# Optimization experiments

Measured on AMD Instinct MI355X. Metric: run time of the kernel, lower is better.

## Reference

```python
import jax, jax.numpy as jnp
import numpy as np

N, I, H = 16, 128, 128
B, T = 16, 512


def setup_inputs() -> dict:
    key = jax.random.key(0)
    ks = jax.random.split(key, 6)
    stdv = 1.0 / np.sqrt(H)
    return {
        "x": jax.random.normal(ks[0], (B, T, N * I), dtype=jnp.float32),
        "h_0": jax.random.normal(ks[1], (1, B, N * H), dtype=jnp.float32),
        "weight_ih": jax.random.uniform(ks[2], (N, 3 * H, I), jnp.float32, -stdv, stdv),
        "weight_hh": jax.random.uniform(ks[3], (N, 3 * H, H), jnp.float32, -stdv, stdv),
        "bias_ih": jax.random.uniform(ks[4], (N, 3 * H), jnp.float32, -stdv, stdv),
        "bias_hh": jax.random.uniform(ks[5], (N, 3 * H), jnp.float32, -stdv, stdv),
    }


def reference(x, h_0, weight_ih, weight_hh, bias_ih, bias_hh):
    # x: [B, T, N*I] (batch_first)
    b, t, _ = x.shape
    xr = x.reshape(b, t, N, I)
    # Pre-compute all input projections: [B, T, N, 3H]
    gates_x = jnp.einsum('btni,ngi->btng', xr, weight_ih) + bias_ih[None, None]
    h0 = h_0[0].reshape(b, N, H)  # [B, N, H]

    def step(h, gx):
        # h: [B, N, H]; gx: [B, N, 3H]
        gates_h = jnp.einsum('bnh,ngh->bng', h, weight_hh) + bias_hh[None]
        gx_r, gx_z, gx_n = jnp.split(gx, 3, axis=-1)
        gh_r, gh_z, gh_n = jnp.split(gates_h, 3, axis=-1)
        r = jax.nn.sigmoid(gx_r + gh_r)
        z = jax.nn.sigmoid(gx_z + gh_z)
        n = jnp.tanh(gx_n + r * gh_n)
        h_new = (1 - z) * n + z * h
        return h_new, h_new

    # scan over time: gates_x -> [T, B, N, 3H]
    h_last, hs = jax.lax.scan(step, h0, jnp.swapaxes(gates_x, 0, 1))
    output = jnp.swapaxes(hs, 0, 1).reshape(b, t, N * H)  # [B, T, N*H]
    h_n = h_last.reshape(1, b, N * H)
    return output, h_n
```

## Files before the change

### kernel.cpp

```cpp
#include <hip/hip_runtime.h>
#include <cstdint>
#include <cmath>

#define N_HEADS 16
#define I_DIM 128
#define H_DIM 128
#define B_SZ 16
#define T_SZ 512
#define G3 384
#define BT (B_SZ * T_SZ)
#define LDW 136
#define OUT_HN_OFFSET ((size_t)B_SZ * T_SZ * (N_HEADS * H_DIM))
#define CHUNK 8
#define NCHUNK (T_SZ / CHUNK)

typedef __attribute__((ext_vector_type(8))) short bf16x8;
typedef __attribute__((ext_vector_type(4))) float f32x4;

static __device__ __forceinline__ unsigned short f2bf(float f) {
  unsigned int u = __float_as_uint(f);
  unsigned int r = (u + 0x7FFFu + ((u >> 16) & 1u)) >> 16;
  return (unsigned short)r;
}
static __device__ __forceinline__ float bf2f(unsigned short s) {
  return __uint_as_float((unsigned int)s << 16);
}
static __device__ __forceinline__ uint2 pack4(float4 v) {
  uint2 p;
  p.x = (unsigned int)f2bf(v.x) | ((unsigned int)f2bf(v.y) << 16);
  p.y = (unsigned int)f2bf(v.z) | ((unsigned int)f2bf(v.w) << 16);
  return p;
}
static __device__ __forceinline__ bf16x8 pack8(float4 a, float4 b) {
  union { uint2 u[2]; bf16x8 v; } r;
  r.u[0] = pack4(a);
  r.u[1] = pack4(b);
  return r.v;
}

__global__ __launch_bounds__(256) void gates_x_mfma(
    const float* __restrict__ x, const float* __restrict__ w_ih,
    const float* __restrict__ b_ih, unsigned short* __restrict__ gates) {
  const int n = blockIdx.z;
  const int grp = blockIdx.x;
  const int tid = threadIdx.x;
  const int wave = tid >> 6;
  const int lane = tid & 63;
  const int m16 = lane & 15;
  const int quad = lane >> 4;

  extern __shared__ __align__(16) unsigned short lds_pool[];
  unsigned short* Ws = lds_pool;
  unsigned short* Xs = lds_pool + G3 * LDW;

  const int xrow = tid >> 2;
  const int xq = tid & 3;

  float4 xf[8];
  {
    const float4* xg =
        (const float4*)(x + (size_t)(grp * 512 + xrow) * 2048 + n * I_DIM) +
        xq * 8;
#pragma unroll
    for (int i = 0; i < 8; ++i) xf[i] = xg[i];
  }

  {
    const float4* wsrc = (const float4*)(w_ih + (size_t)n * G3 * I_DIM);
#pragma unroll
    for (int i = 0; i < 48; ++i) {
      const int idx = i * 256 + tid;
      *(uint2*)&Ws[(idx >> 5) * LDW + (idx & 31) * 4] = pack4(wsrc[idx]);
    }
  }

  float bias[3][8];
#pragma unroll
  for (int gb = 0; gb < 3; ++gb)
#pragma unroll
    for (int j = 0; j < 8; ++j)
      bias[gb][j] = b_ih[n * G3 + gb * 128 + j * 16 + m16];

  for (int tile = 0; tile < 8; ++tile) {
    const int bt0 = grp * 512 + tile * 64;

    __syncthreads();
#pragma unroll
    for (int i = 0; i < 8; ++i)
      *(uint2*)&Xs[xrow * LDW + xq * 32 + i * 4] = pack4(xf[i]);
    __syncthreads();

    if (tile < 7) {
      const float4* xg =
          (const float4*)(x + (size_t)(bt0 + 64 + xrow) * 2048 + n * I_DIM) +
          xq * 8;
#pragma unroll
      for (int i = 0; i < 8; ++i) xf[i] = xg[i];
    }

#pragma unroll
    for (int gb = 0; gb < 3; ++gb) {
      f32x4 acc[8];
#pragma unroll
      for (int j = 0; j < 8; ++j) acc[j] = (f32x4){0.f, 0.f, 0.f, 0.f};

#pragma unroll
      for (int kt = 0; kt < 4; ++kt) {
        const bf16x8 afrag =
            *(const bf16x8*)&Xs[(wave * 16 + m16) * LDW + kt * 32 + quad * 8];
#pragma unroll
        for (int j = 0; j < 8; ++j) {
          const bf16x8 bfrag =
              *(const bf16x8*)&Ws[(gb * 128 + j * 16 + m16) * LDW + kt * 32 +
                                  quad * 8];
          acc[j] = __builtin_amdgcn_mfma_f32_16x16x32_bf16(afrag, bfrag,
                                                           acc[j], 0, 0, 0);
        }
      }

#pragma unroll
      for (int j = 0; j < 8; ++j) {
        const int g = gb * 128 + j * 16 + m16;
#pragma unroll
        for (int r = 0; r < 4; ++r) {
          const int bt = bt0 + wave * 16 + quad * 4 + r;
          gates[((size_t)n * BT + bt) * G3 + g] =
              f2bf(acc[j][r] + bias[gb][j]);
        }
      }
    }
  }
}

__global__ __launch_bounds__(256, 1) void gru_scan_kernel(
    const float* __restrict__ h0, const float* __restrict__ w_hh,
    const float* __restrict__ b_hh, const unsigned short* __restrict__ gates,
    float* __restrict__ out) {
  const int b = blockIdx.x >> 4;
  const int n = blockIdx.x & 15;
  const int tid = threadIdx.x;
  const int wave = tid >> 6;
  const int lane = tid & 63;
  const int m16 = lane & 15;
  const int quad = lane >> 4;

  __shared__ __align__(16) unsigned short h2[2][2][H_DIM];
  __shared__ __align__(16) unsigned short gbuf[2][CHUNK * G3];

  bf16x8 wf[6][4];
  {
    const int cb0 = 2 * wave;
    const int cbs[6] = {cb0, 8 + cb0, 16 + cb0, cb0 + 1, 9 + cb0, 17 + cb0};
#pragma unroll
    for (int j = 0; j < 6; ++j) {
      const int g = cbs[j] * 16 + m16;
      const float4* wr = (const float4*)(w_hh + ((size_t)n * G3 + g) * H_DIM);
#pragma unroll
      for (int kt = 0; kt < 4; ++kt)
        wf[j][kt] = pack8(wr[kt * 8 + quad * 2], wr[kt * 8 + quad * 2 + 1]);
    }
  }

  const bool upd = quad < 2;
  const int elem = wave * 32 + quad * 16 + m16;

  float bh_r = 0.f, bh_z = 0.f, bh_n = 0.f, h_old = 0.f;
  if (upd) {
    bh_r = b_hh[n * G3 + elem];
    bh_z = b_hh[n * G3 + elem + 128];
    bh_n = b_hh[n * G3 + elem + 256];
    h_old = h0[(size_t)b * 2048 + n * H_DIM + elem];
    const unsigned short hh = f2bf(h_old);
    h2[0][0][elem] = hh;
    h2[0][1][elem] = f2bf(h_old - bf2f(hh));
  }

  const unsigned short* gx_base =
      gates + ((size_t)n * BT + (size_t)b * T_SZ) * G3;
  float* out_base = out + (size_t)b * T_SZ * 2048 + n * H_DIM;

  uint2 pf0, pf1, pf2;
  {
    const uint2* gsrc = (const uint2*)gx_base;
    pf0 = gsrc[tid];
    pf1 = gsrc[256 + tid];
    pf2 = gsrc[512 + tid];
    uint2* gd = (uint2*)gbuf[0];
    gd[tid] = pf0;
    gd[256 + tid] = pf1;
    gd[512 + tid] = pf2;
  }
  __syncthreads();

  float oreg[CHUNK];

  for (int c = 0; c < NCHUNK; ++c) {
    const int gb = c & 1;

    if (c + 1 < NCHUNK) {
      const uint2* gsrc =
          (const uint2*)(gx_base + (size_t)(c + 1) * CHUNK * G3);
      pf0 = gsrc[tid];
      pf1 = gsrc[256 + tid];
      pf2 = gsrc[512 + tid];
    }

#pragma unroll
    for (int s = 0; s < CHUNK; ++s) {
      const int rb = s & 1;
      const int wb = rb ^ 1;

      float gxr = 0.f, gxz = 0.f, gxn = 0.f;
      if (upd) {
        const unsigned short* gx = &gbuf[gb][s * G3 + elem];
        gxr = bf2f(gx[0]);
        gxz = bf2f(gx[128]);
        gxn = bf2f(gx[256]);
      }

      f32x4 acc[6];
#pragma unroll
      for (int j = 0; j < 6; ++j) acc[j] = (f32x4){0.f, 0.f, 0.f, 0.f};
#pragma unroll
      for (int kt = 0; kt < 4; ++kt) {
        const bf16x8 av =
            *(const bf16x8*)&h2[rb][m16 & 1][kt * 32 + quad * 8];
#pragma unroll
        for (int j = 0; j < 6; ++j)
          acc[j] = __builtin_amdgcn_mfma_f32_16x16x32_bf16(av, wf[j][kt],
                                                           acc[j], 0, 0, 0);
      }

      const float s0 = acc[0][0] + acc[0][1];
      const float s1 = acc[1][0] + acc[1][1];
      const float s2 = acc[2][0] + acc[2][1];
      const float s3 = acc[3][0] + acc[3][1];
      const float s4 = acc[4][0] + acc[4][1];
      const float s5 = acc[5][0] + acc[5][1];

      if (upd) {
        const float ghr = (quad ? s3 : s0) + bh_r;
        const float ghz = (quad ? s4 : s1) + bh_z;
        const float ghn = (quad ? s5 : s2) + bh_n;
        const float r = 1.f / (1.f + __expf(-(gxr + ghr)));
        const float z = 1.f / (1.f + __expf(-(gxz + ghz)));
        const float targ = gxn + r * ghn;
        const float e2 = __expf(-2.f * fabsf(targ));
        float nn = (1.f - e2) / (1.f + e2);
        nn = (targ < 0.f) ? -nn : nn;
        const float hn = (1.f - z) * nn + z * h_old;
        const unsigned short hh = f2bf(hn);
        h2[wb][0][elem] = hh;
        h2[wb][1][elem] = f2bf(hn - bf2f(hh));
        h_old = hn;
        oreg[s] = hn;
      }

      if (s == CHUNK - 1 && c + 1 < NCHUNK) {
        uint2* gd = (uint2*)gbuf[gb ^ 1];
        gd[tid] = pf0;
        gd[256 + tid] = pf1;
        gd[512 + tid] = pf2;
      }
      __syncthreads();
    }

    if (upd) {
#pragma unroll
      for (int s = 0; s < CHUNK; ++s)
        out_base[(size_t)(c * CHUNK + s) * 2048 + elem] = oreg[s];
    }
  }

  if (upd) {
    out[OUT_HN_OFFSET + (size_t)b * 2048 + n * H_DIM + elem] = h_old;
  }
}

extern "C" void kernel_launch(void* const* d_in, const int* in_sizes, int n_in,
                              void* d_out, int out_size, void* d_ws,
                              size_t ws_size, hipStream_t stream) {
  const float* x    = (const float*)d_in[0];
  const float* h0   = (const float*)d_in[1];
  const float* w_ih = (const float*)d_in[2];
  const float* w_hh = (const float*)d_in[3];
  const float* b_ih = (const float*)d_in[4];
  const float* b_hh = (const float*)d_in[5];
  float* out = (float*)d_out;
  unsigned short* gates = (unsigned short*)d_ws;

  static bool lds_opt_in = false;
  if (!lds_opt_in) {
    (void)hipFuncSetAttribute(reinterpret_cast<const void*>(&gates_x_mfma),
                              hipFuncAttributeMaxDynamicSharedMemorySize,
                              (G3 + 64) * LDW * (int)sizeof(unsigned short));
    lds_opt_in = true;
  }

  dim3 gridA(16, 1, N_HEADS);
  gates_x_mfma<<<gridA, 256, (G3 + 64) * LDW * sizeof(unsigned short),
                 stream>>>(x, w_ih, b_ih, gates);
  gru_scan_kernel<<<256, 256, 0, stream>>>(h0, w_hh, b_hh, gates, out);
}
```

Before: 421.7 us.

## Transpose gate layout to time-major rows and interleave r/z/n in shared memory

```diff
diff --git a/kernel.cpp b/kernel.cpp
--- a/kernel.cpp
+++ b/kernel.cpp
@@ -121,12 +121,13 @@
 #pragma unroll
       for (int j = 0; j < 8; ++j) {
         const int g = gb * 128 + j * 16 + m16;
-#pragma unroll
-        for (int r = 0; r < 4; ++r) {
-          const int bt = bt0 + wave * 16 + quad * 4 + r;
-          gates[((size_t)n * BT + bt) * G3 + g] =
-              f2bf(acc[j][r] + bias[gb][j]);
-        }
+        float4 v;
+        v.x = acc[j][0] + bias[gb][j];
+        v.y = acc[j][1] + bias[gb][j];
+        v.z = acc[j][2] + bias[gb][j];
+        v.w = acc[j][3] + bias[gb][j];
+        const int bt = bt0 + wave * 16 + quad * 4;
+        *(uint2*)&gates[((size_t)n * G3 + g) * BT + bt] = pack4(v);
       }
     }
   }
@@ -145,7 +146,7 @@
   const int quad = lane >> 4;
 
   __shared__ __align__(16) unsigned short h2[2][2][H_DIM];
-  __shared__ __align__(16) unsigned short gbuf[2][CHUNK * G3];
+  __shared__ __align__(16) unsigned short gbuf[2][CHUNK * 512];
 
   bf16x8 wf[6][4];
   {
@@ -175,34 +176,38 @@
     h2[0][1][elem] = f2bf(h_old - bf2f(hh));
   }
 
-  const unsigned short* gx_base =
-      gates + ((size_t)n * BT + (size_t)b * T_SZ) * G3;
+  const size_t grow0 = ((size_t)n * G3 + tid) * BT + (size_t)b * T_SZ;
+  const size_t grow1 = ((size_t)n * G3 + 256 + tid) * BT + (size_t)b * T_SZ;
+
+  auto scatter = [&](unsigned short* buf, int g, uint4 v) {
+    unsigned short* d = buf + (g & 127) * 4 + (g >> 7);
+    d[0]    = (unsigned short)v.x;
+    d[512]  = (unsigned short)(v.x >> 16);
+    d[1024] = (unsigned short)v.y;
+    d[1536] = (unsigned short)(v.y >> 16);
+    d[2048] = (unsigned short)v.z;
+    d[2560] = (unsigned short)(v.z >> 16);
+    d[3072] = (unsigned short)v.w;
+    d[3584] = (unsigned short)(v.w >> 16);
+  };
+
+  uint4 pfA, pfB;
+  pfA = *(const uint4*)(gates + grow0);
+  if (tid < 128) pfB = *(const uint4*)(gates + grow1);
+  scatter(gbuf[0], tid, pfA);
+  if (tid < 128) scatter(gbuf[0], 256 + tid, pfB);
+  __syncthreads();
+
   float* out_base = out + (size_t)b * T_SZ * 2048 + n * H_DIM;
-
-  uint2 pf0, pf1, pf2;
-  {
-    const uint2* gsrc = (const uint2*)gx_base;
-    pf0 = gsrc[tid];
-    pf1 = gsrc[256 + tid];
-    pf2 = gsrc[512 + tid];
-    uint2* gd = (uint2*)gbuf[0];
-    gd[tid] = pf0;
-    gd[256 + tid] = pf1;
-    gd[512 + tid] = pf2;
-  }
-  __syncthreads();
-
   float oreg[CHUNK];
 
   for (int c = 0; c < NCHUNK; ++c) {
     const int gb = c & 1;
 
     if (c + 1 < NCHUNK) {
-      const uint2* gsrc =
-          (const uint2*)(gx_base + (size_t)(c + 1) * CHUNK * G3);
-      pf0 = gsrc[tid];
-      pf1 = gsrc[256 + tid];
-      pf2 = gsrc[512 + tid];
+      pfA = *(const uint4*)(gates + grow0 + (size_t)(c + 1) * CHUNK);
+      if (tid < 128)
+        pfB = *(const uint4*)(gates + grow1 + (size_t)(c + 1) * CHUNK);
     }
 
 #pragma unroll
@@ -210,44 +215,50 @@
       const int rb = s & 1;
       const int wb = rb ^ 1;
 
-      float gxr = 0.f, gxz = 0.f, gxn = 0.f;
+      uint2 gxu = {0u, 0u};
+      if (upd) gxu = *(const uint2*)&gbuf[gb][s * 512 + elem * 4];
+      const float gxr = __uint_as_float(gxu.x << 16);
+      const float gxz = __uint_as_float(gxu.x & 0xffff0000u);
+      const float gxn = __uint_as_float(gxu.y << 16);
+
+      const unsigned short* hsrc = &h2[rb][m16 & 1][0];
+      const bf16x8 av0 = *(const bf16x8*)&hsrc[0 * 32 + quad * 8];
+      const bf16x8 av1 = *(const bf16x8*)&hsrc[1 * 32 + quad * 8];
+      const bf16x8 av2 = *(const bf16x8*)&hsrc[2 * 32 + quad * 8];
+      const bf16x8 av3 = *(const bf16x8*)&hsrc[3 * 32 + quad * 8];
+
+      f32x4 acc[6];
+#pragma unroll
+      for (int j = 0; j < 6; ++j) acc[j] = (f32x4){0.f, 0.f, 0.f, 0.f};
+#pragma unroll
+      for (int j = 0; j < 6; ++j)
+        acc[j] = __builtin_amdgcn_mfma_f32_16x16x32_bf16(av0, wf[j][0],
+                                                         acc[j], 0, 0, 0);
+#pragma unroll
+      for (int j = 0; j < 6; ++j)
+        acc[j] = __builtin_amdgcn_mfma_f32_16x16x32_bf16(av1, wf[j][1],
+                                                         acc[j], 0, 0, 0);
+#pragma unroll
+      for (int j = 0; j < 6; ++j)
+        acc[j] = __builtin_amdgcn_mfma_f32_16x16x32_bf16(av2, wf[j][2],
+                                                         acc[j], 0, 0, 0);
+#pragma unroll
+      for (int j = 0; j < 6; ++j)
+        acc[j] = __builtin_amdgcn_mfma_f32_16x16x32_bf16(av3, wf[j][3],
+                                                         acc[j], 0, 0, 0);
+
       if (upd) {
-        const unsigned short* gx = &gbuf[gb][s * G3 + elem];
-        gxr = bf2f(gx[0]);
-        gxz = bf2f(gx[128]);
-        gxn = bf2f(gx[256]);
-      }
-
-      f32x4 acc[6];
-#pragma unroll
-      for (int j = 0; j < 6; ++j) acc[j] = (f32x4){0.f, 0.f, 0.f, 0.f};
-#pragma unroll
-      for (int kt = 0; kt < 4; ++kt) {
-        const bf16x8 av =
-            *(const bf16x8*)&h2[rb][m16 & 1][kt * 32 + quad * 8];
-#pragma unroll
-        for (int j = 0; j < 6; ++j)
-          acc[j] = __builtin_amdgcn_mfma_f32_16x16x32_bf16(av, wf[j][kt],
-                                                           acc[j], 0, 0, 0);
-      }
-
-      const float s0 = acc[0][0] + acc[0][1];
-      const float s1 = acc[1][0] + acc[1][1];
-      const float s2 = acc[2][0] + acc[2][1];
-      const float s3 = acc[3][0] + acc[3][1];
-      const float s4 = acc[4][0] + acc[4][1];
-      const float s5 = acc[5][0] + acc[5][1];
-
-      if (upd) {
-        const float ghr = (quad ? s3 : s0) + bh_r;
-        const float ghz = (quad ? s4 : s1) + bh_z;
-        const float ghn = (quad ? s5 : s2) + bh_n;
+        const float ghr =
+            (quad ? acc[3][0] + acc[3][1] : acc[0][0] + acc[0][1]) + bh_r;
+        const float ghz =
+            (quad ? acc[4][0] + acc[4][1] : acc[1][0] + acc[1][1]) + bh_z;
+        const float ghn =
+            (quad ? acc[5][0] + acc[5][1] : acc[2][0] + acc[2][1]) + bh_n;
         const float r = 1.f / (1.f + __expf(-(gxr + ghr)));
         const float z = 1.f / (1.f + __expf(-(gxz + ghz)));
         const float targ = gxn + r * ghn;
-        const float e2 = __expf(-2.f * fabsf(targ));
-        float nn = (1.f - e2) / (1.f + e2);
-        nn = (targ < 0.f) ? -nn : nn;
+        const float rt = 1.f / (1.f + __expf(-2.f * targ));
+        const float nn = 2.f * rt - 1.f;
         const float hn = (1.f - z) * nn + z * h_old;
         const unsigned short hh = f2bf(hn);
         h2[wb][0][elem] = hh;
@@ -257,10 +268,8 @@
       }
 
       if (s == CHUNK - 1 && c + 1 < NCHUNK) {
-        uint2* gd = (uint2*)gbuf[gb ^ 1];
-        gd[tid] = pf0;
-        gd[256 + tid] = pf1;
-        gd[512 + tid] = pf2;
+        scatter(gbuf[gb ^ 1], tid, pfA);
+        if (tid < 128) scatter(gbuf[gb ^ 1], 256 + tid, pfB);
       }
       __syncthreads();
     }
```

Measured after the change: 422.7 us. Within noise of the previous version (+0.3%).

## Warp-specialize GRU scan: 8 compute waves plus a producer wave for loads/stores

Applied to the files above, without the earlier changes.

```diff
diff --git a/kernel.cpp b/kernel.cpp
--- a/kernel.cpp
+++ b/kernel.cpp
@@ -13,6 +13,7 @@
 #define OUT_HN_OFFSET ((size_t)B_SZ * T_SZ * (N_HEADS * H_DIM))
 #define CHUNK 8
 #define NCHUNK (T_SZ / CHUNK)
+#define HPAD 160
 
 typedef __attribute__((ext_vector_type(8))) short bf16x8;
 typedef __attribute__((ext_vector_type(4))) float f32x4;
@@ -132,7 +133,7 @@
   }
 }
 
-__global__ __launch_bounds__(256, 1) void gru_scan_kernel(
+__global__ __launch_bounds__(576, 1) void gru_scan_kernel(
     const float* __restrict__ h0, const float* __restrict__ w_hh,
     const float* __restrict__ b_hh, const unsigned short* __restrict__ gates,
     float* __restrict__ out) {
@@ -144,15 +145,19 @@
   const int m16 = lane & 15;
   const int quad = lane >> 4;
 
-  __shared__ __align__(16) unsigned short h2[2][2][H_DIM];
-  __shared__ __align__(16) unsigned short gbuf[2][CHUNK * G3];
-
-  bf16x8 wf[6][4];
-  {
-    const int cb0 = 2 * wave;
-    const int cbs[6] = {cb0, 8 + cb0, 16 + cb0, cb0 + 1, 9 + cb0, 17 + cb0};
-#pragma unroll
-    for (int j = 0; j < 6; ++j) {
+  __shared__ __align__(16) unsigned short h2[2][2][HPAD];
+  __shared__ __align__(16) unsigned short gbuf[2][CHUNK * 512];
+  __shared__ __align__(16) float obuf[2][CHUNK][H_DIM];
+
+  const bool is_comp = wave < 8;
+  const bool upd = is_comp && (quad == 0);
+  const int elem = (is_comp ? wave * 16 : 0) + m16;
+
+  bf16x8 wf[3][4];
+  if (is_comp) {
+    const int cbs[3] = {wave, 8 + wave, 16 + wave};
+#pragma unroll
+    for (int j = 0; j < 3; ++j) {
       const int g = cbs[j] * 16 + m16;
       const float4* wr = (const float4*)(w_hh + ((size_t)n * G3 + g) * H_DIM);
 #pragma unroll
@@ -160,9 +165,6 @@
         wf[j][kt] = pack8(wr[kt * 8 + quad * 2], wr[kt * 8 + quad * 2 + 1]);
     }
   }
-
-  const bool upd = quad < 2;
-  const int elem = wave * 32 + quad * 16 + m16;
 
   float bh_r = 0.f, bh_z = 0.f, bh_n = 0.f, h_old = 0.f;
   if (upd) {
@@ -179,30 +181,59 @@
       gates + ((size_t)n * BT + (size_t)b * T_SZ) * G3;
   float* out_base = out + (size_t)b * T_SZ * 2048 + n * H_DIM;
 
-  uint2 pf0, pf1, pf2;
-  {
-    const uint2* gsrc = (const uint2*)gx_base;
-    pf0 = gsrc[tid];
-    pf1 = gsrc[256 + tid];
-    pf2 = gsrc[512 + tid];
-    uint2* gd = (uint2*)gbuf[0];
-    gd[tid] = pf0;
-    gd[256 + tid] = pf1;
-    gd[512 + tid] = pf2;
+  auto scatter6 = [&](unsigned short* buf, const uint4* v) {
+#pragma unroll
+    for (int j = 0; j < 6; ++j) {
+      const int k = j * 64 + lane;
+      const int s = k / 48;
+      const int g0 = (k - s * 48) * 8;
+      unsigned short* d = buf + s * 512;
+      const unsigned int w[4] = {v[j].x, v[j].y, v[j].z, v[j].w};
+#pragma unroll
+      for (int i = 0; i < 8; ++i) {
+        const int g = g0 + i;
+        d[(g & 127) * 4 + (g >> 7)] =
+            (unsigned short)((i & 1) ? (w[i >> 1] >> 16) : w[i >> 1]);
+      }
+    }
+  };
+
+  uint4 pfv[6];
+  if (!is_comp) {
+    uint4 c0[6];
+#pragma unroll
+    for (int j = 0; j < 6; ++j)
+      c0[j] = ((const uint4*)gx_base)[j * 64 + lane];
+    scatter6(gbuf[0], c0);
+#pragma unroll
+    for (int j = 0; j < 6; ++j)
+      pfv[j] = ((const uint4*)(gx_base + (size_t)CHUNK * G3))[j * 64 + lane];
   }
   __syncthreads();
-
-  float oreg[CHUNK];
 
   for (int c = 0; c < NCHUNK; ++c) {
     const int gb = c & 1;
 
-    if (c + 1 < NCHUNK) {
-      const uint2* gsrc =
-          (const uint2*)(gx_base + (size_t)(c + 1) * CHUNK * G3);
-      pf0 = gsrc[tid];
-      pf1 = gsrc[256 + tid];
-      pf2 = gsrc[512 + tid];
+    if (!is_comp) {
+      if (c >= 1) {
+        const int ob = (c - 1) & 1;
+        const int s = lane >> 3;
+        const int col = (lane & 7) * 16;
+        const float4* src = (const float4*)&obuf[ob][s][col];
+        const float4 v0 = src[0], v1 = src[1], v2 = src[2], v3 = src[3];
+        float* dst = out_base + (size_t)((c - 1) * CHUNK + s) * 2048 + col;
+        *(float4*)&dst[0] = v0;
+        *(float4*)&dst[4] = v1;
+        *(float4*)&dst[8] = v2;
+        *(float4*)&dst[12] = v3;
+      }
+      if (c + 1 < NCHUNK) scatter6(gbuf[gb ^ 1], pfv);
+      if (c + 2 < NCHUNK) {
+        const unsigned short* gch = gx_base + (size_t)(c + 2) * CHUNK * G3;
+#pragma unroll
+        for (int j = 0; j < 6; ++j)
+          pfv[j] = ((const uint4*)gch)[j * 64 + lane];
+      }
     }
 
 #pragma unroll
@@ -211,67 +242,79 @@
       const int wb = rb ^ 1;
 
       float gxr = 0.f, gxz = 0.f, gxn = 0.f;
-      if (upd) {
-        const unsigned short* gx = &gbuf[gb][s * G3 + elem];
-        gxr = bf2f(gx[0]);
-        gxz = bf2f(gx[128]);
-        gxn = bf2f(gx[256]);
-      }
-
-      f32x4 acc[6];
-#pragma unroll
-      for (int j = 0; j < 6; ++j) acc[j] = (f32x4){0.f, 0.f, 0.f, 0.f};
-#pragma unroll
-      for (int kt = 0; kt < 4; ++kt) {
-        const bf16x8 av =
-            *(const bf16x8*)&h2[rb][m16 & 1][kt * 32 + quad * 8];
-#pragma unroll
-        for (int j = 0; j < 6; ++j)
-          acc[j] = __builtin_amdgcn_mfma_f32_16x16x32_bf16(av, wf[j][kt],
-                                                           acc[j], 0, 0, 0);
-      }
-
-      const float s0 = acc[0][0] + acc[0][1];
-      const float s1 = acc[1][0] + acc[1][1];
-      const float s2 = acc[2][0] + acc[2][1];
-      const float s3 = acc[3][0] + acc[3][1];
-      const float s4 = acc[4][0] + acc[4][1];
-      const float s5 = acc[5][0] + acc[5][1];
-
-      if (upd) {
-        const float ghr = (quad ? s3 : s0) + bh_r;
-        const float ghz = (quad ? s4 : s1) + bh_z;
-        const float ghn = (quad ? s5 : s2) + bh_n;
-        const float r = 1.f / (1.f + __expf(-(gxr + ghr)));
-        const float z = 1.f / (1.f + __expf(-(gxz + ghz)));
-        const float targ = gxn + r * ghn;
-        const float e2 = __expf(-2.f * fabsf(targ));
-        float nn = (1.f - e2) / (1.f + e2);
-        nn = (targ < 0.f) ? -nn : nn;
-        const float hn = (1.f - z) * nn + z * h_old;
-        const unsigned short hh = f2bf(hn);
-        h2[wb][0][elem] = hh;
-        h2[wb][1][elem] = f2bf(hn - bf2f(hh));
-        h_old = hn;
-        oreg[s] = hn;
-      }
-
-      if (s == CHUNK - 1 && c + 1 < NCHUNK) {
-        uint2* gd = (uint2*)gbuf[gb ^ 1];
-        gd[tid] = pf0;
-        gd[256 + tid] = pf1;
-        gd[512 + tid] = pf2;
+      bf16x8 av0, av1, av2, av3;
+      if (is_comp) {
+        if (upd) {
+          const uint2 gxu = *(const uint2*)&gbuf[gb][s * 512 + elem * 4];
+          gxr = __uint_as_float(gxu.x << 16);
+          gxz = __uint_as_float(gxu.x & 0xffff0000u);
+          gxn = __uint_as_float(gxu.y << 16);
+        }
+        const unsigned short* hsrc = &h2[rb][m16 & 1][0];
+        av0 = *(const bf16x8*)&hsrc[0 * 32 + quad * 8];
+        av1 = *(const bf16x8*)&hsrc[1 * 32 + quad * 8];
+        av2 = *(const bf16x8*)&hsrc[2 * 32 + quad * 8];
+        av3 = *(const bf16x8*)&hsrc[3 * 32 + quad * 8];
+
+        f32x4 acc[3][4];
+#pragma unroll
+        for (int j = 0; j < 3; ++j)
+#pragma unroll
+          for (int kt = 0; kt < 4; ++kt) acc[j][kt] = (f32x4){0.f, 0.f, 0.f, 0.f};
+#pragma unroll
+        for (int j = 0; j < 3; ++j) {
+          acc[j][0] = __builtin_amdgcn_mfma_f32_16x16x32_bf16(av0, wf[j][0],
+                                                              acc[j][0], 0, 0, 0);
+          acc[j][1] = __builtin_amdgcn_mfma_f32_16x16x32_bf16(av1, wf[j][1],
+                                                              acc[j][1], 0, 0, 0);
+          acc[j][2] = __builtin_amdgcn_mfma_f32_16x16x32_bf16(av2, wf[j][2],
+                                                              acc[j][2], 0, 0, 0);
+          acc[j][3] = __builtin_amdgcn_mfma_f32_16x16x32_bf16(av3, wf[j][3],
+                                                              acc[j][3], 0, 0, 0);
+        }
+
+        if (upd) {
+          const float ghr = ((acc[0][0][0] + acc[0][1][0]) +
+                             (acc[0][2][0] + acc[0][3][0])) +
+                            ((acc[0][0][1] + acc[0][1][1]) +
+                             (acc[0][2][1] + acc[0][3][1])) + bh_r;
+          const float ghz = ((acc[1][0][0] + acc[1][1][0]) +
+                             (acc[1][2][0] + acc[1][3][0])) +
+                            ((acc[1][0][1] + acc[1][1][1]) +
+                             (acc[1][2][1] + acc[1][3][1])) + bh_z;
+          const float ghn = ((acc[2][0][0] + acc[2][1][0]) +
+                             (acc[2][2][0] + acc[2][3][0])) +
+                            ((acc[2][0][1] + acc[2][1][1]) +
+                             (acc[2][2][1] + acc[2][3][1])) + bh_n;
+          const float r = 1.f / (1.f + __expf(-(gxr + ghr)));
+          const float z = 1.f / (1.f + __expf(-(gxz + ghz)));
+          const float targ = gxn + r * ghn;
+          const float rt = 1.f / (1.f + __expf(-2.f * targ));
+          const float nn = 2.f * rt - 1.f;
+          const float hn = (1.f - z) * nn + z * h_old;
+          const unsigned short hh = f2bf(hn);
+          h2[wb][0][elem] = hh;
+          h2[wb][1][elem] = f2bf(hn - bf2f(hh));
+          h_old = hn;
+          obuf[gb][s][elem] = hn;
+        }
       }
       __syncthreads();
     }
-
-    if (upd) {
-#pragma unroll
-      for (int s = 0; s < CHUNK; ++s)
-        out_base[(size_t)(c * CHUNK + s) * 2048 + elem] = oreg[s];
-    }
-  }
-
+  }
+
+  if (!is_comp) {
+    const int ob = (NCHUNK - 1) & 1;
+    const int s = lane >> 3;
+    const int col = (lane & 7) * 16;
+    const float4* src = (const float4*)&obuf[ob][s][col];
+    const float4 v0 = src[0], v1 = src[1], v2 = src[2], v3 = src[3];
+    float* dst = out_base + (size_t)((NCHUNK - 1) * CHUNK + s) * 2048 + col;
+    *(float4*)&dst[0] = v0;
+    *(float4*)&dst[4] = v1;
+    *(float4*)&dst[8] = v2;
+    *(float4*)&dst[12] = v3;
+  }
   if (upd) {
     out[OUT_HN_OFFSET + (size_t)b * 2048 + n * H_DIM + elem] = h_old;
   }
@@ -300,5 +343,5 @@
   dim3 gridA(16, 1, N_HEADS);
   gates_x_mfma<<<gridA, 256, (G3 + 64) * LDW * sizeof(unsigned short),
                  stream>>>(x, w_ih, b_ih, gates);
-  gru_scan_kernel<<<256, 256, 0, stream>>>(h0, w_hh, b_hh, gates, out);
-}
+  gru_scan_kernel<<<256, 576, 0, stream>>>(h0, w_hh, b_hh, gates, out);
+}
```

Result: slower. 463.7 us (+10.0%).
